# Optimization experiments

Hardware: AMD Instinct MI355X
Metric: run time of the kernel (lower is better)

Reference implementation:

```python
import jax, jax.numpy as jnp
import numpy as np

B, N = 65536, 128  # batch of point clouds, points per cloud

def setup_inputs() -> dict:
    key = jax.random.key(0)
    k1, k2 = jax.random.split(key)
    x = jax.random.normal(k1, (B, N, 3), dtype=jnp.float32)
    y = jax.random.normal(k2, (B, N, 3), dtype=jnp.float32)
    return {"x": x, "y": y}

def reference(x, y):
    # zero-center both point clouds
    xc = x - x.mean(axis=-2, keepdims=True)
    yc = y - y.mean(axis=-2, keepdims=True)
    # batched 3x3 covariance: C[..., j, k] = sum_i xc[..., i, j] * yc[..., i, k]
    C = jnp.einsum('...ij,...ik->...jk', xc, yc)
    # torch.linalg.svd returns (U, S, Vh); original code names Vh as V and forms R = U @ Vh
    U, _, Vh = jnp.linalg.svd(C)
    R = jnp.einsum('...ij,...jk->...ik', U, Vh)
    x_aligned = jnp.einsum('...ij,...jk->...ik', xc, R)
    # mean square deviation over all batch, point, and coordinate dims
    return jnp.mean((x_aligned - yc) ** 2)
```

## Files before the change

kernel.cpp:

```cpp
#include <hip/hip_runtime.h>
#include <math.h>


#define NPTS 128

__device__ __forceinline__ float xsum(float v, int m) {
    return v + __shfl_xor(v, m);
}

__global__ __launch_bounds__(256, 4) void kabsch_kernel(
        const float* __restrict__ x, const float* __restrict__ y,
        float* __restrict__ out, float scale) {
    const int tid  = threadIdx.x;
    const int lane = tid & 63;
    const int wave = tid >> 6;
    const int g    = lane >> 3;
    const int sub  = lane & 7;
    const int b    = blockIdx.x * 32 + wave * 8 + g;

    const float4* xb = (const float4*)(x + (size_t)b * (NPTS * 3)) + sub * 3;
    const float4* yb = (const float4*)(y + (size_t)b * (NPTS * 3)) + sub * 3;

    float sx0=0.f,sx1=0.f,sx2=0.f, sy0=0.f,sy1=0.f,sy2=0.f;
    float qx=0.f, qy=0.f;
    float c00=0.f,c01=0.f,c02=0.f,c10=0.f,c11=0.f,c12=0.f,c20=0.f,c21=0.f,c22=0.f;

#define ACC(px0,px1,px2,py0,py1,py2) do {                                    \
        sx0+=(px0); sx1+=(px1); sx2+=(px2);                                  \
        sy0+=(py0); sy1+=(py1); sy2+=(py2);                                  \
        qx = fmaf((px0),(px0),fmaf((px1),(px1),fmaf((px2),(px2),qx)));       \
        qy = fmaf((py0),(py0),fmaf((py1),(py1),fmaf((py2),(py2),qy)));       \
        c00=fmaf((px0),(py0),c00); c01=fmaf((px0),(py1),c01); c02=fmaf((px0),(py2),c02); \
        c10=fmaf((px1),(py0),c10); c11=fmaf((px1),(py1),c11); c12=fmaf((px1),(py2),c12); \
        c20=fmaf((px2),(py0),c20); c21=fmaf((px2),(py1),c21); c22=fmaf((px2),(py2),c22); \
    } while (0)

    float4 bx[4][3], by[4][3];
    #pragma unroll
    for (int s = 0; s < 2; ++s) {
        bx[s][0] = xb[s*24 + 0]; bx[s][1] = xb[s*24 + 1]; bx[s][2] = xb[s*24 + 2];
        by[s][0] = yb[s*24 + 0]; by[s][1] = yb[s*24 + 1]; by[s][2] = yb[s*24 + 2];
    }
    #pragma unroll
    for (int s = 0; s < 4; ++s) {
        if (s + 2 < 4) {
            const int t = s + 2;
            bx[t][0] = xb[t*24 + 0]; bx[t][1] = xb[t*24 + 1]; bx[t][2] = xb[t*24 + 2];
            by[t][0] = yb[t*24 + 0]; by[t][1] = yb[t*24 + 1]; by[t][2] = yb[t*24 + 2];
        }
        const float4 q0 = bx[s][0], q1 = bx[s][1], q2 = bx[s][2];
        const float4 r0 = by[s][0], r1 = by[s][1], r2 = by[s][2];
        ACC(q0.x, q0.y, q0.z,  r0.x, r0.y, r0.z);
        ACC(q0.w, q1.x, q1.y,  r0.w, r1.x, r1.y);
        ACC(q1.z, q1.w, q2.x,  r1.z, r1.w, r2.x);
        ACC(q2.y, q2.z, q2.w,  r2.y, r2.z, r2.w);
    }
#undef ACC

    #pragma unroll
    for (int m = 1; m <= 4; m <<= 1) {
        sx0=xsum(sx0,m); sx1=xsum(sx1,m); sx2=xsum(sx2,m);
        sy0=xsum(sy0,m); sy1=xsum(sy1,m); sy2=xsum(sy2,m);
        qx =xsum(qx ,m); qy =xsum(qy ,m);
        c00=xsum(c00,m); c01=xsum(c01,m); c02=xsum(c02,m);
        c10=xsum(c10,m); c11=xsum(c11,m); c12=xsum(c12,m);
        c20=xsum(c20,m); c21=xsum(c21,m); c22=xsum(c22,m);
    }

    const float invN = 1.0f / (float)NPTS;
    float C00 = c00 - sx0*sy0*invN, C01 = c01 - sx0*sy1*invN, C02 = c02 - sx0*sy2*invN;
    float C10 = c10 - sx1*sy0*invN, C11 = c11 - sx1*sy1*invN, C12 = c12 - sx1*sy2*invN;
    float C20 = c20 - sx2*sy0*invN, C21 = c21 - sx2*sy1*invN, C22 = c22 - sx2*sy2*invN;
    float Sx = qx - (sx0*sx0 + sx1*sx1 + sx2*sx2) * invN;
    float Sy = qy - (sy0*sy0 + sy1*sy1 + sy2*sy2) * invN;

    float a00 = C00*C00 + C10*C10 + C20*C20;
    float a01 = C00*C01 + C10*C11 + C20*C21;
    float a02 = C00*C02 + C10*C12 + C20*C22;
    float a11 = C01*C01 + C11*C11 + C21*C21;
    float a12 = C01*C02 + C11*C12 + C21*C22;
    float a22 = C02*C02 + C12*C12 + C22*C22;

    float q = (a00 + a11 + a22) * (1.0f / 3.0f);
    float b00 = a00 - q, b11 = a11 - q, b22 = a22 - q;
    float p2 = (b00*b00 + b11*b11 + b22*b22
                + 2.0f * (a01*a01 + a02*a02 + a12*a12)) * (1.0f / 6.0f);
    float p = sqrtf(fmaxf(p2, 0.0f));
    float detB = b00 * (b11*b22 - a12*a12)
               - a01 * (a01*b22 - a12*a02)
               + a02 * (a01*a12 - b11*a02);
    float p3 = p * p * p;
    float r = (p3 > 1e-30f) ? (0.5f * detB / p3) : 0.0f;
    r = fminf(1.0f, fmaxf(-1.0f, r));
    float phi = acosf(r) * (1.0f / 3.0f);
    float two_p = 2.0f * p;
    float l1 = q + two_p * cosf(phi);
    float l3 = q + two_p * cosf(phi + 2.0943951023931953f);
    float l2 = 3.0f * q - l1 - l3;
    float nuc = sqrtf(fmaxf(l1, 0.0f)) + sqrtf(fmaxf(l2, 0.0f)) + sqrtf(fmaxf(l3, 0.0f));

    float term = Sx + Sy - 2.0f * nuc;

    term += __shfl_xor(term, 8);
    term += __shfl_xor(term, 16);
    term += __shfl_xor(term, 32);

    __shared__ float wsum[4];
    if (lane == 0) wsum[wave] = term;
    __syncthreads();
    if (tid == 0) {
        float t = (wsum[0] + wsum[1] + wsum[2] + wsum[3]) * scale;
        atomicAdd(out, t);
    }
}

extern "C" void kernel_launch(void* const* d_in, const int* in_sizes, int n_in,
                              void* d_out, int out_size, void* d_ws, size_t ws_size,
                              hipStream_t stream) {
    const float* x = (const float*)d_in[0];
    const float* y = (const float*)d_in[1];
    float* out = (float*)d_out;

    const int B = in_sizes[0] / (NPTS * 3);
    const float scale = 1.0f / ((float)B * (float)NPTS * 3.0f);

    hipMemsetAsync(out, 0, sizeof(float), stream);
    const int blocks = B / 32;
    kabsch_kernel<<<blocks, 256, 0, stream>>>(x, y, out, scale);
}
```

Measured before the change: 216.1 us.

## Use 16 threads per cloud with contiguous 8-point loads issued upfront

Each point cloud is now handled by 16 lanes instead of 8. Each lane loads 8 contiguous points (six float4 per input) all at once rather than 16 strided points in a software-pipelined loop. This doubles the number of blocks and the parallelism available to hide memory latency, at the cost of one more shuffle-reduction stage and twice as many threads repeating the per-cloud eigenvalue math. The contiguous per-lane chunks also change the coalescing pattern.

```diff
diff --git a/kernel.cpp b/kernel.cpp
--- a/kernel.cpp
+++ b/kernel.cpp
@@ -3,6 +3,7 @@
 
 
 #define NPTS 128
+#define BPB 16
 
 __device__ __forceinline__ float xsum(float v, int m) {
     return v + __shfl_xor(v, m);
@@ -14,12 +15,17 @@
     const int tid  = threadIdx.x;
     const int lane = tid & 63;
     const int wave = tid >> 6;
-    const int g    = lane >> 3;
-    const int sub  = lane & 7;
-    const int b    = blockIdx.x * 32 + wave * 8 + g;
+    const int sub  = tid & 15;
+    const int b    = blockIdx.x * BPB + (tid >> 4);
 
-    const float4* xb = (const float4*)(x + (size_t)b * (NPTS * 3)) + sub * 3;
-    const float4* yb = (const float4*)(y + (size_t)b * (NPTS * 3)) + sub * 3;
+    const float4* xb = (const float4*)(x + (size_t)b * (NPTS * 3)) + sub * 6;
+    const float4* yb = (const float4*)(y + (size_t)b * (NPTS * 3)) + sub * 6;
+
+    const float4 q0 = xb[0], q1 = xb[1], q2 = xb[2];
+    const float4 q3 = xb[3], q4 = xb[4], q5 = xb[5];
+    const float4 r0 = yb[0], r1 = yb[1], r2 = yb[2];
+    const float4 r3 = yb[3], r4 = yb[4], r5 = yb[5];
+    asm volatile("" ::: "memory");
 
     float sx0=0.f,sx1=0.f,sx2=0.f, sy0=0.f,sy1=0.f,sy2=0.f;
     float qx=0.f, qy=0.f;
@@ -35,30 +41,18 @@
         c20=fmaf((px2),(py0),c20); c21=fmaf((px2),(py1),c21); c22=fmaf((px2),(py2),c22); \
     } while (0)
 
-    float4 bx[4][3], by[4][3];
-    #pragma unroll
-    for (int s = 0; s < 2; ++s) {
-        bx[s][0] = xb[s*24 + 0]; bx[s][1] = xb[s*24 + 1]; bx[s][2] = xb[s*24 + 2];
-        by[s][0] = yb[s*24 + 0]; by[s][1] = yb[s*24 + 1]; by[s][2] = yb[s*24 + 2];
-    }
-    #pragma unroll
-    for (int s = 0; s < 4; ++s) {
-        if (s + 2 < 4) {
-            const int t = s + 2;
-            bx[t][0] = xb[t*24 + 0]; bx[t][1] = xb[t*24 + 1]; bx[t][2] = xb[t*24 + 2];
-            by[t][0] = yb[t*24 + 0]; by[t][1] = yb[t*24 + 1]; by[t][2] = yb[t*24 + 2];
-        }
-        const float4 q0 = bx[s][0], q1 = bx[s][1], q2 = bx[s][2];
-        const float4 r0 = by[s][0], r1 = by[s][1], r2 = by[s][2];
-        ACC(q0.x, q0.y, q0.z,  r0.x, r0.y, r0.z);
-        ACC(q0.w, q1.x, q1.y,  r0.w, r1.x, r1.y);
-        ACC(q1.z, q1.w, q2.x,  r1.z, r1.w, r2.x);
-        ACC(q2.y, q2.z, q2.w,  r2.y, r2.z, r2.w);
-    }
+    ACC(q0.x, q0.y, q0.z,  r0.x, r0.y, r0.z);
+    ACC(q0.w, q1.x, q1.y,  r0.w, r1.x, r1.y);
+    ACC(q1.z, q1.w, q2.x,  r1.z, r1.w, r2.x);
+    ACC(q2.y, q2.z, q2.w,  r2.y, r2.z, r2.w);
+    ACC(q3.x, q3.y, q3.z,  r3.x, r3.y, r3.z);
+    ACC(q3.w, q4.x, q4.y,  r3.w, r4.x, r4.y);
+    ACC(q4.z, q4.w, q5.x,  r4.z, r4.w, r5.x);
+    ACC(q5.y, q5.z, q5.w,  r5.y, r5.z, r5.w);
 #undef ACC
 
     #pragma unroll
-    for (int m = 1; m <= 4; m <<= 1) {
+    for (int m = 1; m <= 8; m <<= 1) {
         sx0=xsum(sx0,m); sx1=xsum(sx1,m); sx2=xsum(sx2,m);
         sy0=xsum(sy0,m); sy1=xsum(sy1,m); sy2=xsum(sy2,m);
         qx =xsum(qx ,m); qy =xsum(qy ,m);
@@ -101,7 +95,6 @@
 
     float term = Sx + Sy - 2.0f * nuc;
 
-    term += __shfl_xor(term, 8);
     term += __shfl_xor(term, 16);
     term += __shfl_xor(term, 32);
 
@@ -125,6 +118,6 @@
     const float scale = 1.0f / ((float)B * (float)NPTS * 3.0f);
 
     hipMemsetAsync(out, 0, sizeof(float), stream);
-    const int blocks = B / 32;
+    const int blocks = B / BPB;
     kabsch_kernel<<<blocks, 256, 0, stream>>>(x, y, out, scale);
 }
```

Measured after the change: 222.0 us. 1.03x slower.

## Stage point chunks through double-buffered LDS with coalesced global loads

Applied to the files above, without the earlier changes.

Each block now loads 32-point chunks of its 32 clouds with fully contiguous float4 global loads into a double-buffered LDS staging area, then each thread reads its own points from LDS. The old per-thread strided loads had each group of 8 lanes reading a separate cloud. Coalesced streaming and prefetching the next chunk are meant to improve DRAM efficiency. In exchange it adds about 51KB of LDS per block, four block-wide barriers, and the min-blocks launch bound is dropped, which may lower occupancy.

```diff
diff --git a/kernel.cpp b/kernel.cpp
--- a/kernel.cpp
+++ b/kernel.cpp
@@ -3,23 +3,45 @@
 
 
 #define NPTS 128
+#define BPB 32
+#define CPTS 32
+#define NCH (NPTS / CPTS)
+#define CHB (CPTS * 12)
+#define BSTRIDE 400
+#define ARR_BYTES (BPB * BSTRIDE)
+#define BUF_BYTES (2 * ARR_BYTES)
 
 __device__ __forceinline__ float xsum(float v, int m) {
     return v + __shfl_xor(v, m);
 }
 
-__global__ __launch_bounds__(256, 4) void kabsch_kernel(
+__global__ __launch_bounds__(256) void kabsch_kernel(
         const float* __restrict__ x, const float* __restrict__ y,
         float* __restrict__ out, float scale) {
+    __shared__ char lds[2 * BUF_BYTES];
+    __shared__ float wsum[4];
+
     const int tid  = threadIdx.x;
     const int lane = tid & 63;
     const int wave = tid >> 6;
-    const int g    = lane >> 3;
     const int sub  = lane & 7;
-    const int b    = blockIdx.x * 32 + wave * 8 + g;
+    const int gb   = tid >> 3;
 
-    const float4* xb = (const float4*)(x + (size_t)b * (NPTS * 3)) + sub * 3;
-    const float4* yb = (const float4*)(y + (size_t)b * (NPTS * 3)) + sub * 3;
+    const size_t b0 = (size_t)blockIdx.x * BPB;
+    const char* xB0 = (const char*)(x + b0 * (NPTS * 3));
+    const char* yB0 = (const char*)(y + b0 * (NPTS * 3));
+
+    const char* srcb[6];
+    int         ldso[6];
+    #pragma unroll
+    for (int jj = 0; jj < 6; ++jj) {
+        const int jx  = (jj < 3) ? jj : jj - 3;
+        const int i   = tid * 16 + jx * 4096;
+        const int bt  = i / CHB;
+        const int rem = i - bt * CHB;
+        srcb[jj] = ((jj < 3) ? xB0 : yB0) + (size_t)bt * (NPTS * 12) + rem;
+        ldso[jj] = ((jj < 3) ? 0 : ARR_BYTES) + bt * BSTRIDE + rem;
+    }
 
     float sx0=0.f,sx1=0.f,sx2=0.f, sy0=0.f,sy1=0.f,sy2=0.f;
     float qx=0.f, qy=0.f;
@@ -35,25 +57,45 @@
         c20=fmaf((px2),(py0),c20); c21=fmaf((px2),(py1),c21); c22=fmaf((px2),(py2),c22); \
     } while (0)
 
-    float4 bx[4][3], by[4][3];
+    {
+        float4 st[6];
+        #pragma unroll
+        for (int jj = 0; jj < 6; ++jj) st[jj] = *(const float4*)(srcb[jj]);
+        #pragma unroll
+        for (int jj = 0; jj < 6; ++jj) *(float4*)(lds + ldso[jj]) = st[jj];
+    }
+
     #pragma unroll
-    for (int s = 0; s < 2; ++s) {
-        bx[s][0] = xb[s*24 + 0]; bx[s][1] = xb[s*24 + 1]; bx[s][2] = xb[s*24 + 2];
-        by[s][0] = yb[s*24 + 0]; by[s][1] = yb[s*24 + 1]; by[s][2] = yb[s*24 + 2];
-    }
-    #pragma unroll
-    for (int s = 0; s < 4; ++s) {
-        if (s + 2 < 4) {
-            const int t = s + 2;
-            bx[t][0] = xb[t*24 + 0]; bx[t][1] = xb[t*24 + 1]; bx[t][2] = xb[t*24 + 2];
-            by[t][0] = yb[t*24 + 0]; by[t][1] = yb[t*24 + 1]; by[t][2] = yb[t*24 + 2];
+    for (int c = 0; c < NCH; ++c) {
+        __syncthreads();
+        const int rb = (c & 1) ? BUF_BYTES : 0;
+        const int wb = (c & 1) ? 0 : BUF_BYTES;
+
+        float4 st[6];
+        if (c + 1 < NCH) {
+            #pragma unroll
+            for (int jj = 0; jj < 6; ++jj)
+                st[jj] = *(const float4*)(srcb[jj] + (c + 1) * CHB);
         }
-        const float4 q0 = bx[s][0], q1 = bx[s][1], q2 = bx[s][2];
-        const float4 r0 = by[s][0], r1 = by[s][1], r2 = by[s][2];
+
+        const char* xp = lds + rb + gb * BSTRIDE + sub * 48;
+        const char* yp = xp + ARR_BYTES;
+        const float4 q0 = *(const float4*)(xp);
+        const float4 q1 = *(const float4*)(xp + 16);
+        const float4 q2 = *(const float4*)(xp + 32);
+        const float4 r0 = *(const float4*)(yp);
+        const float4 r1 = *(const float4*)(yp + 16);
+        const float4 r2 = *(const float4*)(yp + 32);
         ACC(q0.x, q0.y, q0.z,  r0.x, r0.y, r0.z);
         ACC(q0.w, q1.x, q1.y,  r0.w, r1.x, r1.y);
         ACC(q1.z, q1.w, q2.x,  r1.z, r1.w, r2.x);
         ACC(q2.y, q2.z, q2.w,  r2.y, r2.z, r2.w);
+
+        if (c + 1 < NCH) {
+            #pragma unroll
+            for (int jj = 0; jj < 6; ++jj)
+                *(float4*)(lds + wb + ldso[jj]) = st[jj];
+        }
     }
 #undef ACC
 
@@ -105,7 +147,6 @@
     term += __shfl_xor(term, 16);
     term += __shfl_xor(term, 32);
 
-    __shared__ float wsum[4];
     if (lane == 0) wsum[wave] = term;
     __syncthreads();
     if (tid == 0) {
@@ -125,6 +166,6 @@
     const float scale = 1.0f / ((float)B * (float)NPTS * 3.0f);
 
     hipMemsetAsync(out, 0, sizeof(float), stream);
-    const int blocks = B / 32;
+    const int blocks = B / BPB;
     kabsch_kernel<<<blocks, 256, 0, stream>>>(x, y, out, scale);
 }
```

Result: no change. 214.8 us (-0.6%).
